# Kernel tuning notes

Hardware: AMD Instinct MI355X
Metric: run time of the kernel (lower is better)

The kernel has to match this reference:

```python
import jax, jax.numpy as jnp
import numpy as np

B, S, D_MODEL, N_HEADS, D_HEAD = 2, 2048, 512, 8, 64
AMBIENT_K = -1.0
EPS = 1e-7


def log_map_origin(x, K):
    """Lorentz log map at origin, curvature K<0. x: (..., d+1) -> (..., d)."""
    c = -K
    sc = jnp.sqrt(c)
    x_t = x[..., :1]
    x_s = x[..., 1:]
    nrm = jnp.maximum(jnp.linalg.norm(x_s, axis=-1, keepdims=True), EPS)
    theta = jnp.arccosh(jnp.maximum(sc * x_t, 1.0 + EPS)) / sc  # geodesic distance
    return theta * x_s / nrm


def exp_map_batched(u, K_vals):
    """Per-head Lorentz exp map at origin. u: (B,S,H,dh), K_vals: (H,) negative.
    Returns (B,S,H,dh+1) with time component first."""
    c = (-K_vals)[None, None, :, None]          # (1,1,H,1)
    sc = jnp.sqrt(c)
    n = jnp.maximum(jnp.linalg.norm(u, axis=-1, keepdims=True), EPS)
    t = jnp.cosh(sc * n) / sc                   # time component
    s = jnp.sinh(sc * n) / (sc * n) * u         # space components
    return jnp.concatenate([t, s], axis=-1)


def setup_inputs() -> dict:
    key = jax.random.key(0)
    k_x, k_q, k_k, k_v, k_o = jax.random.split(key, 5)
    # Lorentz points on the K=-1 manifold: x_t = sqrt(1 + |x_s|^2)
    x_s = 0.5 * jax.random.normal(k_x, (B, S, D_MODEL), dtype=jnp.float32)
    x_t = jnp.sqrt(1.0 + jnp.sum(x_s * x_s, axis=-1, keepdims=True))
    x = jnp.concatenate([x_t, x_s], axis=-1)    # (B, S, d_model+1)
    scale = 1.0 / np.sqrt(D_MODEL)
    W_q = scale * jax.random.normal(k_q, (D_MODEL, N_HEADS * D_HEAD), dtype=jnp.float32)
    W_k = scale * jax.random.normal(k_k, (D_MODEL, N_HEADS * D_HEAD), dtype=jnp.float32)
    W_v = scale * jax.random.normal(k_v, (D_MODEL, N_HEADS * D_HEAD), dtype=jnp.float32)
    W_o = scale * jax.random.normal(k_o, (N_HEADS * D_HEAD, D_MODEL), dtype=jnp.float32)
    log_abs_K = jnp.zeros((N_HEADS,), dtype=jnp.float32)  # init_K = -1 -> log(1) = 0
    return {"x": x, "W_q": W_q, "W_k": W_k, "W_v": W_v, "W_o": W_o,
            "log_abs_K": log_abs_K}


def reference(x, W_q, W_k, W_v, W_o, log_abs_K):
    b, s, _ = x.shape
    K_vals = -jnp.exp(log_abs_K)                            # (H,) negative curvatures
    x_eu = log_map_origin(x, AMBIENT_K)                     # (B,S,D)
    Q = (x_eu @ W_q).reshape(b, s, N_HEADS, D_HEAD)
    Kp = (x_eu @ W_k).reshape(b, s, N_HEADS, D_HEAD)
    V = (x_eu @ W_v).reshape(b, s, N_HEADS, D_HEAD)
    Q_hyp = exp_map_batched(Q, K_vals).transpose(0, 2, 1, 3)   # (B,H,S,dh+1)
    K_hyp = exp_map_batched(Kp, K_vals).transpose(0, 2, 1, 3)
    V = V.transpose(0, 2, 1, 3)                                # (B,H,S,dh)
    Q_t, Q_s = Q_hyp[..., 0], Q_hyp[..., 1:]
    K_t, K_s = K_hyp[..., 0], K_hyp[..., 1:]
    # Lorentzian inner product: -q_t k_t + <q_s, k_s>
    lorentz_ip = (jnp.einsum('bhqd,bhkd->bhqk', Q_s, K_s)
                  - jnp.einsum('bhq,bhk->bhqk', Q_t, K_t))
    abs_K = jnp.exp(log_abs_K)[None, :, None, None]
    scores = abs_K * (-lorentz_ip) / np.sqrt(D_HEAD)           # (B,H,S,S)
    causal = jnp.triu(jnp.ones((s, s), dtype=bool), k=1)[None, None]
    scores = jnp.where(causal, -jnp.inf, scores)
    attn = jax.nn.softmax(scores, axis=-1)
    out = jnp.einsum('bhqk,bhkd->bhqd', attn, V)               # (B,H,S,dh)
    out = out.transpose(0, 2, 1, 3).reshape(b, s, N_HEADS * D_HEAD)
    return out @ W_o                                           # (B,S,D)
```

## Files before the change

kernel.cpp:

```cpp
#include <hip/hip_runtime.h>
#include <math.h>

#define S_LEN 2048
#define B_SZ 2
#define NH 8
#define DH 64
#define DM 512
#define MROWS 4096

typedef __attribute__((ext_vector_type(8))) short s16x8;
typedef __attribute__((ext_vector_type(4))) float fx4;
typedef __attribute__((ext_vector_type(16))) float fx16;
typedef __attribute__((ext_vector_type(4))) int ix4;

__device__ inline short f2bf(float x){
  unsigned u = __float_as_uint(x);
  u = (u + 0x7FFFu + ((u >> 16) & 1u)) >> 16;
  return (short)u;
}

__device__ inline fx4 mfma16(s16x8 a, s16x8 b, fx4 c){
  return __builtin_amdgcn_mfma_f32_16x16x32_bf16(a, b, c, 0, 0, 0);
}
__device__ inline fx16 mfma32(s16x8 a, s16x8 b, fx16 c){
  return __builtin_amdgcn_mfma_f32_32x32x16_bf16(a, b, c, 0, 0, 0);
}
__device__ inline int cvtpk(float a, float b){
  int r; asm("v_cvt_pk_bf16_f32 %0, %1, %2" : "=v"(r) : "v"(a), "v"(b)); return r;
}

#define GLL16(g, l) __builtin_amdgcn_global_load_lds((const __attribute__((address_space(1))) void*)(g), (__attribute__((address_space(3))) void*)(l), 16, 0, 0)
#define GLL4(g, l)  __builtin_amdgcn_global_load_lds((const __attribute__((address_space(1))) void*)(g), (__attribute__((address_space(3))) void*)(l), 4, 0, 0)

__global__ __launch_bounds__(256) void prep_kernel(const float* __restrict__ W0,
                                                   const float* __restrict__ W1,
                                                   const float* __restrict__ W2,
                                                   const float* __restrict__ W3,
                                                   short* __restrict__ Wt,
                                                   const float* __restrict__ x,
                                                   short* __restrict__ xeu){
  __shared__ short tile[64][66];
  __shared__ float s4[4];
  int bid = blockIdx.x;
  int t = threadIdx.x;
  if (bid < 256){
    int z = bid >> 6, rem = bid & 63;
    const float* W = (z == 0) ? W0 : (z == 1) ? W1 : (z == 2) ? W2 : W3;
    short* Wtz = Wt + (size_t)z * DM * DM;
    int n0 = (rem & 7) * 64, k0 = (rem >> 3) * 64;
    int nl = t & 63;
    #pragma unroll
    for (int p = 0; p < 16; ++p){
      int kl = (t >> 6) + p * 4;
      tile[kl][nl] = f2bf(W[(size_t)(k0 + kl) * DM + n0 + nl]);
    }
    __syncthreads();
    int kl2 = t & 63;
    #pragma unroll
    for (int p = 0; p < 16; ++p){
      int nl2 = (t >> 6) + p * 4;
      Wtz[(size_t)(n0 + nl2) * DM + k0 + kl2] = tile[kl2][nl2];
    }
  } else {
    int row = 2 * (bid - 256) + (t >> 7);
    int tl = t & 127;
    const float* xr = x + (size_t)row * (DM + 1);
    float v[4]; float ss = 0.f;
    #pragma unroll
    for (int j = 0; j < 4; ++j){
      v[j] = xr[1 + tl + 128 * j];
      ss += v[j] * v[j];
    }
    #pragma unroll
    for (int off = 1; off < 64; off <<= 1) ss += __shfl_xor(ss, off);
    if ((t & 63) == 0) s4[t >> 6] = ss;
    __syncthreads();
    int g2 = t >> 7;
    float tot = s4[2 * g2] + s4[2 * g2 + 1];
    float nrm = sqrtf(tot);
    float xt = xr[0];
    float theta = acoshf(fmaxf(xt, 1.0f + 1e-7f));
    float scl = theta / fmaxf(nrm, 1e-7f);
    #pragma unroll
    for (int j = 0; j < 4; ++j)
      xeu[(size_t)row * DM + tl + 128 * j] = f2bf(scl * v[j]);
  }
}

__global__ __launch_bounds__(256, 3) void gemm_fused_kernel(const short* __restrict__ A,
                                                            const short* __restrict__ Bt,
                                                            const float* __restrict__ labsK,
                                                            float* __restrict__ Qt,
                                                            short* __restrict__ Qs,
                                                            float* __restrict__ Kt,
                                                            short* __restrict__ Ks,
                                                            short* __restrict__ Vt){
  __shared__ __attribute__((aligned(16))) short Asm[2][128 * 64];
  __shared__ __attribute__((aligned(16))) short Bsm[2][64 * 64];
  __shared__ float nrm2s[2][128];
  const int K = DM;
  int z = blockIdx.z;
  int h = blockIdx.y;
  int n0 = h * 64, m0 = blockIdx.x * 128;
  int t = threadIdx.x;
  int w = t >> 6, lane = t & 63;
  int wm = w >> 1, wn = w & 1;
  int lg = lane >> 4, lr = lane & 15;
  const short* Btz = Bt + (size_t)z * K * DM;

  int aoff[4]; const short* asrcp[4];
  int boff[2]; const short* bsrcp[2];
  #pragma unroll
  for (int j = 0; j < 4; ++j){
    int ch = t + 256 * j;
    int r = ch >> 3, c = ch & 7;
    aoff[j] = ch * 8;
    asrcp[j] = A + (size_t)(m0 + r) * K + 8 * (c ^ (r & 7));
  }
  #pragma unroll
  for (int j = 0; j < 2; ++j){
    int ch = t + 256 * j;
    int r = ch >> 3, c = ch & 7;
    boff[j] = ch * 8;
    bsrcp[j] = Btz + (size_t)(n0 + r) * K + 8 * (c ^ (r & 7));
  }

  {
    short* ab = &Asm[0][0]; short* bb = &Bsm[0][0];
    #pragma unroll
    for (int j = 0; j < 4; ++j) GLL16(asrcp[j], ab + aoff[j]);
    #pragma unroll
    for (int j = 0; j < 2; ++j) GLL16(bsrcp[j], bb + boff[j]);
  }

  fx4 acc[4][2] = {};
  for (int ks = 0; ks < 8; ++ks){
    asm volatile("s_waitcnt vmcnt(0)" ::: "memory");
    __builtin_amdgcn_s_barrier();
    if (ks < 7){
      int nb = (ks + 1) & 1;
      short* ab = &Asm[nb][0]; short* bb = &Bsm[nb][0];
      int kk = (ks + 1) * 64;
      #pragma unroll
      for (int j = 0; j < 4; ++j) GLL16(asrcp[j] + kk, ab + aoff[j]);
      #pragma unroll
      for (int j = 0; j < 2; ++j) GLL16(bsrcp[j] + kk, bb + boff[j]);
    }
    int buf = ks & 1;
    s16x8 af[4][2], bf[2][2];
    #pragma unroll
    for (int mi = 0; mi < 4; ++mi){
      int row = wm * 64 + mi * 16 + lr;
      #pragma unroll
      for (int s = 0; s < 2; ++s)
        af[mi][s] = *(const s16x8*)&Asm[buf][row * 64 + ((4 * s + lg) ^ (row & 7)) * 8];
    }
    #pragma unroll
    for (int ni = 0; ni < 2; ++ni){
      int row = wn * 32 + ni * 16 + lr;
      #pragma unroll
      for (int s = 0; s < 2; ++s)
        bf[ni][s] = *(const s16x8*)&Bsm[buf][row * 64 + ((4 * s + lg) ^ (row & 7)) * 8];
    }
    __builtin_amdgcn_s_setprio(1);
    #pragma unroll
    for (int s = 0; s < 2; ++s)
      #pragma unroll
      for (int mi = 0; mi < 4; ++mi)
        #pragma unroll
        for (int ni = 0; ni < 2; ++ni)
          acc[mi][ni] = mfma16(af[mi][s], bf[ni][s], acc[mi][ni]);
    __builtin_amdgcn_s_setprio(0);
  }

  if (z < 2){
    #pragma unroll
    for (int mi = 0; mi < 4; ++mi)
      #pragma unroll
      for (int r = 0; r < 4; ++r){
        float prt = acc[mi][0][r] * acc[mi][0][r] + acc[mi][1][r] * acc[mi][1][r];
        prt += __shfl_xor(prt, 1);
        prt += __shfl_xor(prt, 2);
        prt += __shfl_xor(prt, 4);
        prt += __shfl_xor(prt, 8);
        if (lr == 0) nrm2s[wn][wm * 64 + mi * 16 + 4 * lg + r] = prt;
      }
    __syncthreads();
    float c  = __expf(labsK[h]);
    float sc = sqrtf(c);
    float invsc = __frcp_rn(sc);
    float a  = 0.125f * c * 1.4426950408889634f;
    float tmul = (z == 0) ? a : 1.0f;
    float vmul = (z == 0) ? -a : 1.0f;
    float* Tt = (z == 0) ? Qt : Kt;
    short* Ts = (z == 0) ? Qs : Ks;
    #pragma unroll
    for (int mi = 0; mi < 4; ++mi)
      #pragma unroll
      for (int r = 0; r < 4; ++r){
        int row_local = wm * 64 + mi * 16 + 4 * lg + r;
        float full = nrm2s[0][row_local] + nrm2s[1][row_local];
        float n = fmaxf(sqrtf(full), 1e-7f);
        float arg = sc * n;
        float e = __expf(arg), ei = __frcp_rn(e);
        float tval = tmul * 0.5f * (e + ei) * invsc;
        float vscl = vmul * 0.5f * (e - ei) * __frcp_rn(arg);
        int grow = m0 + row_local;
        int b = grow >> 11, s = grow & (S_LEN - 1);
        size_t bhs = ((size_t)(b * NH + h) * S_LEN + s);
        if (lr == 0) Tt[bhs] = tval;
        #pragma unroll
        for (int ni = 0; ni < 2; ++ni)
          Ts[bhs * DH + wn * 32 + ni * 16 + lr] = f2bf(vscl * acc[mi][ni][r]);
      }
  } else {
    short* vt = (short*)&Asm[0][0];
    __syncthreads();
    #pragma unroll
    for (int mi = 0; mi < 4; ++mi)
      #pragma unroll
      for (int ni = 0; ni < 2; ++ni)
        #pragma unroll
        for (int r = 0; r < 4; ++r){
          int row_local = wm * 64 + mi * 16 + 4 * lg + r;
          int col_local = wn * 32 + ni * 16 + lr;
          vt[col_local * 136 + row_local] = f2bf(acc[mi][ni][r]);
        }
    __syncthreads();
    int d = t >> 2, sseg = (t & 3) * 32;
    int b = m0 >> 11;
    size_t vbase = ((size_t)(b * NH + h) * DH + d) * S_LEN + (m0 & (S_LEN - 1)) + sseg;
    #pragma unroll
    for (int j = 0; j < 4; ++j){
      s16x8 val = *(const s16x8*)&vt[d * 136 + sseg + 8 * j];
      *(s16x8*)(Vt + vbase + 8 * j) = val;
    }
  }
}

__global__ __launch_bounds__(256, 3) void attn_kernel(const short* __restrict__ Qs,
                                                      const float* __restrict__ Qt,
                                                      const short* __restrict__ Ks,
                                                      const float* __restrict__ Kt,
                                                      const short* __restrict__ Vt,
                                                      float* __restrict__ Mpart,
                                                      float* __restrict__ Lpart,
                                                      float* __restrict__ Opart){
  __shared__ __attribute__((aligned(16))) short Ksm[3][4096];
  __shared__ __attribute__((aligned(16))) short Vsm[3][4096];
  __shared__ __attribute__((aligned(16))) float Ktm[3][64];

  int bx = blockIdx.x;
  int bh = bx & 15;
  int id = bx >> 4;
  int g, c;
  if (id < 4)       { g = id;                 c = 0; }
  else if (id < 12) { g = 4 + ((id - 4) >> 1);  c = (id - 4) & 1; }
  else if (id < 24) { int r = id - 12; int q3 = r / 3; g = 8 + q3; c = r - 3 * q3; }
  else              { g = 12 + ((id - 24) >> 2); c = (id - 24) & 3; }
  int kbeg = 512 * c;
  int kend = 512 * c + 512; { int ge = 128 * g + 128; if (ge < kend) kend = ge; }
  int ntc = (kend - kbeg) >> 6;

  int tid = threadIdx.x;
  int w = tid >> 6, lane = tid & 63;
  int l5 = lane & 31, hi = lane >> 5;
  size_t bhS = (size_t)bh * S_LEN;

  const short* Kg  = Ks + bhS * DH;
  const short* Vg  = Vt + (size_t)bh * DH * S_LEN;
  const float* Ktg = Kt + bhS;

  int srow = lane >> 3;
  int scol = ((lane & 7) * 8) ^ (srow << 3);
  const short* kg0 = Kg + (size_t)(kbeg + 16 * w + srow) * DH + scol;
  const short* kg1 = kg0 + 8 * DH;
  const short* vg0 = Vg + (size_t)(16 * w + srow) * S_LEN + kbeg + scol;
  const short* vg1 = vg0 + 8 * S_LEN;
  const float* ktg = Ktg + kbeg + lane;

  int q0w = 128 * g + 32 * w;
  int q   = q0w + l5;
  int qmax = q0w + 31;
  s16x8 qf[4];
  #pragma unroll
  for (int dblk = 0; dblk < 4; ++dblk)
    qf[dblk] = *(const s16x8*)(Qs + (bhS + q) * DH + dblk * 16 + hi * 8);
  float aqt = Qt[bhS + q];

  fx16 acc0, acc1;
  #pragma unroll
  for (int i = 0; i < 16; ++i){ acc0[i] = 0.f; acc1[i] = 0.f; }
  float mrun = 0.f, lrun = 0.f;

  #define STAGE_T(tt, b) { int off_ = (tt) * 64; \
    GLL16(kg0 + (size_t)off_ * DH, &Ksm[b][16 * w * 64]); \
    GLL16(kg1 + (size_t)off_ * DH, &Ksm[b][16 * w * 64 + 512]); \
    GLL16(vg0 + off_, &Vsm[b][16 * w * 64]); \
    GLL16(vg1 + off_, &Vsm[b][16 * w * 64 + 512]); \
    if (w == 3) GLL4(ktg + off_, &Ktm[b][0]); }

  STAGE_T(0, 0);
  if (ntc > 1) STAGE_T(1, 1);

  int buf = 0, sbuf = 2;
  for (int t = 0; t < ntc; ++t){
    int k0 = kbeg + t * 64;
    if (t + 1 < ntc){
      if (w == 3) asm volatile("s_waitcnt vmcnt(5)" ::: "memory");
      else        asm volatile("s_waitcnt vmcnt(4)" ::: "memory");
    } else {
      asm volatile("s_waitcnt vmcnt(0)" ::: "memory");
    }
    __builtin_amdgcn_s_barrier();
    if (t + 2 < ntc) STAGE_T(t + 2, sbuf);

    if (k0 <= qmax){
      fx16 st[2];
      __builtin_amdgcn_s_setprio(1);
      #pragma unroll
      for (int s = 0; s < 2; ++s){
        const short* kb = &Ksm[buf][(32 * s + l5) * 64];
        fx16 z;
        #pragma unroll
        for (int i = 0; i < 16; ++i) z[i] = 0.f;
        #pragma unroll
        for (int dblk = 0; dblk < 4; ++dblk){
          s16x8 kf = *(const s16x8*)(kb + ((16 * dblk + 8 * hi) ^ ((l5 & 7) << 3)));
          z = mfma32(kf, qf[dblk], z);
        }
        st[s] = z;
      }
      __builtin_amdgcn_s_setprio(0);
      float p[2][16];
      #pragma unroll
      for (int s = 0; s < 2; ++s)
        #pragma unroll
        for (int m4 = 0; m4 < 4; ++m4){
          fx4 kt4 = *(const fx4*)&Ktm[buf][32 * s + 8 * m4 + 4 * hi];
          #pragma unroll
          for (int tt = 0; tt < 4; ++tt)
            p[s][4 * m4 + tt] = st[s][4 * m4 + tt] + aqt * kt4[tt];
        }
      if (k0 + 63 > q0w){
        #pragma unroll
        for (int s = 0; s < 2; ++s)
          #pragma unroll
          for (int r = 0; r < 16; ++r){
            int kg2 = k0 + 32 * s + (r & 3) + 8 * (r >> 2) + 4 * hi;
            if (kg2 > q) p[s][r] = -3e38f;
          }
      }
      float v16[16];
      #pragma unroll
      for (int i = 0; i < 16; ++i) v16[i] = fmaxf(p[0][i], p[1][i]);
      #pragma unroll
      for (int i = 0; i < 8; ++i) v16[i] = fmaxf(v16[i], v16[i + 8]);
      #pragma unroll
      for (int i = 0; i < 4; ++i) v16[i] = fmaxf(v16[i], v16[i + 4]);
      float pmax = fmaxf(fmaxf(v16[0], v16[1]), fmaxf(v16[2], v16[3]));
      pmax = fmaxf(pmax, __shfl_xor(pmax, 32));
      if (!__all(pmax <= mrun + 8.f)){
        float mnew = fmaxf(mrun, pmax);
        float scl = __builtin_amdgcn_exp2f(mrun - mnew);
        mrun = mnew;
        lrun *= scl;
        #pragma unroll
        for (int i = 0; i < 16; ++i){ acc0[i] *= scl; acc1[i] *= scl; }
      }
      float sm[16];
      #pragma unroll
      for (int i = 0; i < 16; ++i){
        p[0][i] = __builtin_amdgcn_exp2f(p[0][i] - mrun);
        p[1][i] = __builtin_amdgcn_exp2f(p[1][i] - mrun);
        sm[i] = p[0][i] + p[1][i];
      }
      #pragma unroll
      for (int i = 0; i < 8; ++i) sm[i] += sm[i + 8];
      #pragma unroll
      for (int i = 0; i < 4; ++i) sm[i] += sm[i + 4];
      float rsum = (sm[0] + sm[1]) + (sm[2] + sm[3]);
      rsum += __shfl_xor(rsum, 32);
      lrun += rsum;

      #pragma unroll
      for (int h = 0; h < 4; ++h){
        int s = h >> 1, hb = h & 1;
        int w0 = cvtpk(p[s][8 * hb + 0], p[s][8 * hb + 1]);
        int w1 = cvtpk(p[s][8 * hb + 2], p[s][8 * hb + 3]);
        int w2 = cvtpk(p[s][8 * hb + 4], p[s][8 * hb + 5]);
        int w3 = cvtpk(p[s][8 * hb + 6], p[s][8 * hb + 7]);
        int sdA = hi ? w0 : w2;
        int sdB = hi ? w1 : w3;
        int rcA = __shfl_xor(sdA, 32);
        int rcB = __shfl_xor(sdB, 32);
        ix4 fw;
        fw.x = hi ? rcA : w0; fw.y = hi ? rcB : w1;
        fw.z = hi ? w2 : rcA; fw.w = hi ? w3 : rcB;
        s16x8 pf = __builtin_bit_cast(s16x8, fw);
        const short* vb0 = &Vsm[buf][(l5) * 64 + ((16 * h + 8 * hi) ^ ((l5 & 7) << 3))];
        const short* vb1 = vb0 + 32 * 64;
        s16x8 vf0 = *(const s16x8*)vb0;
        s16x8 vf1 = *(const s16x8*)vb1;
        __builtin_amdgcn_s_setprio(1);
        acc0 = mfma32(vf0, pf, acc0);
        acc1 = mfma32(vf1, pf, acc1);
        __builtin_amdgcn_s_setprio(0);
      }
    }
    buf  = (buf == 2)  ? 0 : buf + 1;
    sbuf = (sbuf == 2) ? 0 : sbuf + 1;
  }

  int slot = ((bh << 4) + g) * 4 + c;
  int qi = 32 * w + l5;
  if (hi == 0){
    Mpart[(size_t)slot * 128 + qi] = mrun;
    Lpart[(size_t)slot * 128 + qi] = lrun;
  }
  float* Op = Opart + (size_t)slot * 8192 + (size_t)qi * 64;
  #pragma unroll
  for (int j = 0; j < 4; ++j){
    fx4 v0, v1;
    #pragma unroll
    for (int i = 0; i < 4; ++i){ v0[i] = acc0[4 * j + i]; v1[i] = acc1[4 * j + i]; }
    *(fx4*)(Op + 8 * j + 4 * hi)      = v0;
    *(fx4*)(Op + 32 + 8 * j + 4 * hi) = v1;
  }
}

__global__ __launch_bounds__(256) void combine_kernel(const float* __restrict__ Mpart,
                                                      const float* __restrict__ Lpart,
                                                      const float* __restrict__ Opart,
                                                      short* __restrict__ Obf){
  int bx = blockIdx.x;
  int bhg = bx & 255;
  int bh = bhg & 15, g = bhg >> 4;
  int qq = bx >> 8;
  int t = threadIdx.x;
  int q = qq * 32 + (t >> 3);
  int oct = t & 7;
  int nch = (g >> 2) + 1;
  int gbase = ((bh << 4) + g) * 4;

  float mc[4], lc[4];
  #pragma unroll
  for (int c = 0; c < 4; ++c){
    mc[c] = Mpart[(size_t)(gbase + c) * 128 + q];
    lc[c] = Lpart[(size_t)(gbase + c) * 128 + q];
    if (c >= nch) mc[c] = -3e38f;
  }
  float M = fmaxf(fmaxf(mc[0], mc[1]), fmaxf(mc[2], mc[3]));
  float wc[4]; float L = 0.f;
  #pragma unroll
  for (int c = 0; c < 4; ++c){
    wc[c] = __builtin_amdgcn_exp2f(mc[c] - M);
    L += wc[c] * lc[c];
  }
  float invL = 1.f / L;
  #pragma unroll
  for (int c = 0; c < 4; ++c) wc[c] *= invL;

  const float* ob = Opart + (size_t)gbase * 8192 + (size_t)q * 64 + oct * 8;
  float accf[8] = {0.f,0.f,0.f,0.f,0.f,0.f,0.f,0.f};
  #pragma unroll
  for (int c = 0; c < 4; ++c){
    fx4 a = *(const fx4*)(ob + (size_t)c * 8192);
    fx4 b = *(const fx4*)(ob + (size_t)c * 8192 + 4);
    #pragma unroll
    for (int k = 0; k < 4; ++k){ accf[k] += wc[c] * a[k]; accf[4 + k] += wc[c] * b[k]; }
  }
  s16x8 pk;
  #pragma unroll
  for (int dd = 0; dd < 8; ++dd) pk[dd] = f2bf(accf[dd]);
  int bb = bh >> 3, hh = bh & 7;
  *(s16x8*)(Obf + ((size_t)bb * S_LEN + 128 * g + q) * DM + hh * DH + oct * 8) = pk;
}

__global__ __launch_bounds__(256, 4) void gemm_o_kernel(const short* __restrict__ A,
                                                        const short* __restrict__ Bt,
                                                        float* __restrict__ C){
  __shared__ __attribute__((aligned(16))) short Asm[2][64 * 64];
  __shared__ __attribute__((aligned(16))) short Bsm[2][64 * 64];
  const int K = DM;
  int n0 = blockIdx.y * 64, m0 = blockIdx.x * 64;
  int t = threadIdx.x;
  int w = t >> 6, lane = t & 63;
  int wm = w >> 1, wn = w & 1;
  int lg = lane >> 4, lr = lane & 15;

  int aoff[2]; const short* asrcp[2];
  int boff[2]; const short* bsrcp[2];
  #pragma unroll
  for (int j = 0; j < 2; ++j){
    int ch = t + 256 * j;
    int r = ch >> 3, c = ch & 7;
    aoff[j] = ch * 8;
    asrcp[j] = A + (size_t)(m0 + r) * K + 8 * (c ^ (r & 7));
    boff[j] = ch * 8;
    bsrcp[j] = Bt + (size_t)(n0 + r) * K + 8 * (c ^ (r & 7));
  }

  {
    short* ab = &Asm[0][0]; short* bb = &Bsm[0][0];
    #pragma unroll
    for (int j = 0; j < 2; ++j){ GLL16(asrcp[j], ab + aoff[j]); GLL16(bsrcp[j], bb + boff[j]); }
  }

  fx4 acc[2][2] = {};
  for (int ks = 0; ks < 8; ++ks){
    asm volatile("s_waitcnt vmcnt(0)" ::: "memory");
    __builtin_amdgcn_s_barrier();
    if (ks < 7){
      int nb = (ks + 1) & 1;
      short* ab = &Asm[nb][0]; short* bb = &Bsm[nb][0];
      int kk = (ks + 1) * 64;
      #pragma unroll
      for (int j = 0; j < 2; ++j){ GLL16(asrcp[j] + kk, ab + aoff[j]); GLL16(bsrcp[j] + kk, bb + boff[j]); }
    }
    int buf = ks & 1;
    s16x8 af[2][2], bf[2][2];
    #pragma unroll
    for (int mi = 0; mi < 2; ++mi){
      int row = wm * 32 + mi * 16 + lr;
      #pragma unroll
      for (int s = 0; s < 2; ++s)
        af[mi][s] = *(const s16x8*)&Asm[buf][row * 64 + ((4 * s + lg) ^ (row & 7)) * 8];
    }
    #pragma unroll
    for (int ni = 0; ni < 2; ++ni){
      int row = wn * 32 + ni * 16 + lr;
      #pragma unroll
      for (int s = 0; s < 2; ++s)
        bf[ni][s] = *(const s16x8*)&Bsm[buf][row * 64 + ((4 * s + lg) ^ (row & 7)) * 8];
    }
    __builtin_amdgcn_s_setprio(1);
    #pragma unroll
    for (int s = 0; s < 2; ++s)
      #pragma unroll
      for (int mi = 0; mi < 2; ++mi)
        #pragma unroll
        for (int ni = 0; ni < 2; ++ni)
          acc[mi][ni] = mfma16(af[mi][s], bf[ni][s], acc[mi][ni]);
    __builtin_amdgcn_s_setprio(0);
  }

  #pragma unroll
  for (int mi = 0; mi < 2; ++mi)
    #pragma unroll
    for (int ni = 0; ni < 2; ++ni)
      #pragma unroll
      for (int r = 0; r < 4; ++r){
        int row = m0 + wm * 32 + mi * 16 + 4 * lg + r;
        int col = n0 + wn * 32 + ni * 16 + lr;
        C[(size_t)row * DM + col] = acc[mi][ni][r];
      }
}

extern "C" void kernel_launch(void* const* d_in, const int* in_sizes, int n_in,
                              void* d_out, int out_size, void* d_ws, size_t ws_size,
                              hipStream_t stream) {
  const float* x     = (const float*)d_in[0];
  const float* Wq    = (const float*)d_in[1];
  const float* Wk    = (const float*)d_in[2];
  const float* Wv    = (const float*)d_in[3];
  const float* Wo    = (const float*)d_in[4];
  const float* labsK = (const float*)d_in[5];

  char* w = (char*)d_ws;
  short* Wt    = (short*)(w);
  short* xeu   = (short*)(w + (2ull  << 20));
  short* Qs    = (short*)(w + (30ull << 20));
  short* Ks    = (short*)(w + (34ull << 20));
  short* Vt    = (short*)(w + (38ull << 20));
  float* Qt    = (float*)(w + (42ull << 20));
  float* Kt    = (float*)(w + (42ull << 20) + (128ull << 10));
  short* Obf   = (short*)(w + (42ull << 20) + (256ull << 10));
  float* Opart = (float*)(w + (48ull << 20));
  float* Mpart = (float*)(w + (80ull << 20));
  float* Lpart = (float*)(w + (81ull << 20));

  prep_kernel<<<dim3(2304), 256, 0, stream>>>(Wq, Wk, Wv, Wo, Wt, x, xeu);

  gemm_fused_kernel<<<dim3(32, 8, 3), 256, 0, stream>>>(
      xeu, Wt, labsK, Qt, Qs, Kt, Ks, Vt);

  attn_kernel<<<dim3(640), 256, 0, stream>>>(
      Qs, Qt, Ks, Kt, Vt, Mpart, Lpart, Opart);

  combine_kernel<<<dim3(1024), 256, 0, stream>>>(Mpart, Lpart, Opart, Obf);

  gemm_o_kernel<<<dim3(64, 8), 256, 0, stream>>>(Obf, Wt + 3 * DM * DM, (float*)d_out);
}
```

Before: 65.86 us.

## Widen QKV GEMM tiles, store normalized bf16 partials, skip combine for single-chunk groups

```diff
diff --git a/kernel.cpp b/kernel.cpp
--- a/kernel.cpp
+++ b/kernel.cpp
@@ -12,11 +12,15 @@
 typedef __attribute__((ext_vector_type(4))) float fx4;
 typedef __attribute__((ext_vector_type(16))) float fx16;
 typedef __attribute__((ext_vector_type(4))) int ix4;
+typedef __attribute__((ext_vector_type(2))) int ix2;
 
 __device__ inline short f2bf(float x){
   unsigned u = __float_as_uint(x);
   u = (u + 0x7FFFu + ((u >> 16) & 1u)) >> 16;
   return (short)u;
+}
+__device__ inline float bf2f(short s){
+  return __uint_as_float(((unsigned)(unsigned short)s) << 16);
 }
 
 __device__ inline fx4 mfma16(s16x8 a, s16x8 b, fx4 c){
@@ -40,7 +44,6 @@
                                                    const float* __restrict__ x,
                                                    short* __restrict__ xeu){
   __shared__ short tile[64][66];
-  __shared__ float s4[4];
   int bid = blockIdx.x;
   int t = threadIdx.x;
   if (bid < 256){
@@ -62,32 +65,29 @@
       Wtz[(size_t)(n0 + nl2) * DM + k0 + kl2] = tile[kl2][nl2];
     }
   } else {
-    int row = 2 * (bid - 256) + (t >> 7);
-    int tl = t & 127;
+    int row = (bid - 256) * 4 + (t >> 6);
+    int lane = t & 63;
     const float* xr = x + (size_t)row * (DM + 1);
-    float v[4]; float ss = 0.f;
-    #pragma unroll
-    for (int j = 0; j < 4; ++j){
-      v[j] = xr[1 + tl + 128 * j];
+    float v[8]; float ss = 0.f;
+    #pragma unroll
+    for (int j = 0; j < 8; ++j){
+      v[j] = xr[1 + lane * 8 + j];
       ss += v[j] * v[j];
     }
     #pragma unroll
     for (int off = 1; off < 64; off <<= 1) ss += __shfl_xor(ss, off);
-    if ((t & 63) == 0) s4[t >> 6] = ss;
-    __syncthreads();
-    int g2 = t >> 7;
-    float tot = s4[2 * g2] + s4[2 * g2 + 1];
-    float nrm = sqrtf(tot);
+    float nrm = sqrtf(ss);
     float xt = xr[0];
     float theta = acoshf(fmaxf(xt, 1.0f + 1e-7f));
     float scl = theta / fmaxf(nrm, 1e-7f);
-    #pragma unroll
-    for (int j = 0; j < 4; ++j)
-      xeu[(size_t)row * DM + tl + 128 * j] = f2bf(scl * v[j]);
-  }
-}
-
-__global__ __launch_bounds__(256, 3) void gemm_fused_kernel(const short* __restrict__ A,
+    s16x8 pk;
+    #pragma unroll
+    for (int j = 0; j < 8; ++j) pk[j] = f2bf(scl * v[j]);
+    *(s16x8*)(xeu + (size_t)row * DM + lane * 8) = pk;
+  }
+}
+
+__global__ __launch_bounds__(256, 2) void gemm_fused_kernel(const short* __restrict__ A,
                                                             const short* __restrict__ Bt,
                                                             const float* __restrict__ labsK,
                                                             float* __restrict__ Qt,
@@ -95,72 +95,65 @@
                                                             float* __restrict__ Kt,
                                                             short* __restrict__ Ks,
                                                             short* __restrict__ Vt){
-  __shared__ __attribute__((aligned(16))) short Asm[2][128 * 64];
-  __shared__ __attribute__((aligned(16))) short Bsm[2][64 * 64];
-  __shared__ float nrm2s[2][128];
+  __shared__ __attribute__((aligned(16))) short Stage[4][8192];
   const int K = DM;
   int z = blockIdx.z;
-  int h = blockIdx.y;
-  int n0 = h * 64, m0 = blockIdx.x * 128;
+  int hp = blockIdx.y;
+  int n0 = hp * 128, m0 = blockIdx.x * 128;
   int t = threadIdx.x;
   int w = t >> 6, lane = t & 63;
   int wm = w >> 1, wn = w & 1;
   int lg = lane >> 4, lr = lane & 15;
   const short* Btz = Bt + (size_t)z * K * DM;
 
-  int aoff[4]; const short* asrcp[4];
-  int boff[2]; const short* bsrcp[2];
+  int coff[4]; const short* asrcp[4]; const short* bsrcp[4];
   #pragma unroll
   for (int j = 0; j < 4; ++j){
     int ch = t + 256 * j;
     int r = ch >> 3, c = ch & 7;
-    aoff[j] = ch * 8;
-    asrcp[j] = A + (size_t)(m0 + r) * K + 8 * (c ^ (r & 7));
-  }
-  #pragma unroll
-  for (int j = 0; j < 2; ++j){
-    int ch = t + 256 * j;
-    int r = ch >> 3, c = ch & 7;
-    boff[j] = ch * 8;
+    coff[j] = ch * 8;
+    asrcp[j] = A   + (size_t)(m0 + r) * K + 8 * (c ^ (r & 7));
     bsrcp[j] = Btz + (size_t)(n0 + r) * K + 8 * (c ^ (r & 7));
   }
 
-  {
-    short* ab = &Asm[0][0]; short* bb = &Bsm[0][0];
-    #pragma unroll
-    for (int j = 0; j < 4; ++j) GLL16(asrcp[j], ab + aoff[j]);
-    #pragma unroll
-    for (int j = 0; j < 2; ++j) GLL16(bsrcp[j], bb + boff[j]);
-  }
-
-  fx4 acc[4][2] = {};
+  #pragma unroll
+  for (int j = 0; j < 4; ++j){
+    GLL16(asrcp[j], &Stage[0][coff[j]]);
+    GLL16(bsrcp[j], &Stage[2][coff[j]]);
+  }
+
+  fx4 acc[4][4] = {};
+  for (int ks = 0; ks < 4; ++ks){
+    ;
+    break;
+  }
   for (int ks = 0; ks < 8; ++ks){
     asm volatile("s_waitcnt vmcnt(0)" ::: "memory");
     __builtin_amdgcn_s_barrier();
     if (ks < 7){
       int nb = (ks + 1) & 1;
-      short* ab = &Asm[nb][0]; short* bb = &Bsm[nb][0];
       int kk = (ks + 1) * 64;
       #pragma unroll
-      for (int j = 0; j < 4; ++j) GLL16(asrcp[j] + kk, ab + aoff[j]);
-      #pragma unroll
-      for (int j = 0; j < 2; ++j) GLL16(bsrcp[j] + kk, bb + boff[j]);
+      for (int j = 0; j < 4; ++j){
+        GLL16(asrcp[j] + kk, &Stage[nb][coff[j]]);
+        GLL16(bsrcp[j] + kk, &Stage[2 + nb][coff[j]]);
+      }
     }
     int buf = ks & 1;
-    s16x8 af[4][2], bf[2][2];
+    s16x8 af[4][2], bf[4][2];
     #pragma unroll
     for (int mi = 0; mi < 4; ++mi){
       int row = wm * 64 + mi * 16 + lr;
       #pragma unroll
       for (int s = 0; s < 2; ++s)
-        af[mi][s] = *(const s16x8*)&Asm[buf][row * 64 + ((4 * s + lg) ^ (row & 7)) * 8];
-    }
-    #pragma unroll
-    for (int ni = 0; ni < 2; ++ni){
-      int row = wn * 32 + ni * 16 + lr;
+        af[mi][s] = *(const s16x8*)&Stage[buf][row * 64 + ((4 * s + lg) ^ (row & 7)) * 8];
+    }
+    #pragma unroll
+    for (int ni = 0; ni < 4; ++ni){
+      int row = wn * 64 + ni * 16 + lr;
       #pragma unroll
       for (int s = 0; s < 2; ++s)
-        bf[ni][s] = *(const s16x8*)&Bsm[buf][row * 64 + ((4 * s + lg) ^ (row & 7)) * 8];
+        bf[ni][s] = *(const s16x8*)&Stage[2 + buf][row * 64 + ((4 * s + lg) ^ (row & 7)) * 8];
     }
     __builtin_amdgcn_s_setprio(1);
     #pragma unroll
@@ -168,24 +161,13 @@
       #pragma unroll
       for (int mi = 0; mi < 4; ++mi)
         #pragma unroll
-        for (int ni = 0; ni < 2; ++ni)
+        for (int ni = 0; ni < 4; ++ni)
           acc[mi][ni] = mfma16(af[mi][s], bf[ni][s], acc[mi][ni]);
     __builtin_amdgcn_s_setprio(0);
   }
 
+  int h = hp * 2 + wn;
   if (z < 2){
-    #pragma unroll
-    for (int mi = 0; mi < 4; ++mi)
-      #pragma unroll
-      for (int r = 0; r < 4; ++r){
-        float prt = acc[mi][0][r] * acc[mi][0][r] + acc[mi][1][r] * acc[mi][1][r];
-        prt += __shfl_xor(prt, 1);
-        prt += __shfl_xor(prt, 2);
-        prt += __shfl_xor(prt, 4);
-        prt += __shfl_xor(prt, 8);
-        if (lr == 0) nrm2s[wn][wm * 64 + mi * 16 + 4 * lg + r] = prt;
-      }
-    __syncthreads();
     float c  = __expf(labsK[h]);
     float sc = sqrtf(c);
     float invsc = __frcp_rn(sc);
@@ -198,42 +180,43 @@
     for (int mi = 0; mi < 4; ++mi)
       #pragma unroll
       for (int r = 0; r < 4; ++r){
-        int row_local = wm * 64 + mi * 16 + 4 * lg + r;
-        float full = nrm2s[0][row_local] + nrm2s[1][row_local];
-        float n = fmaxf(sqrtf(full), 1e-7f);
+        float prt = 0.f;
+        #pragma unroll
+        for (int ni = 0; ni < 4; ++ni) prt += acc[mi][ni][r] * acc[mi][ni][r];
+        prt += __shfl_xor(prt, 1);
+        prt += __shfl_xor(prt, 2);
+        prt += __shfl_xor(prt, 4);
+        prt += __shfl_xor(prt, 8);
+        float n = fmaxf(sqrtf(prt), 1e-7f);
         float arg = sc * n;
         float e = __expf(arg), ei = __frcp_rn(e);
         float tval = tmul * 0.5f * (e + ei) * invsc;
         float vscl = vmul * 0.5f * (e - ei) * __frcp_rn(arg);
-        int grow = m0 + row_local;
+        int grow = m0 + wm * 64 + mi * 16 + 4 * lg + r;
         int b = grow >> 11, s = grow & (S_LEN - 1);
         size_t bhs = ((size_t)(b * NH + h) * S_LEN + s);
         if (lr == 0) Tt[bhs] = tval;
         #pragma unroll
-        for (int ni = 0; ni < 2; ++ni)
-          Ts[bhs * DH + wn * 32 + ni * 16 + lr] = f2bf(vscl * acc[mi][ni][r]);
+        for (int ni = 0; ni < 4; ++ni)
+          Ts[bhs * DH + ni * 16 + lr] = f2bf(vscl * acc[mi][ni][r]);
       }
   } else {
-    short* vt = (short*)&Asm[0][0];
     __syncthreads();
+    short* vt = &Stage[0][0] + w * 4352;
     #pragma unroll
     for (int mi = 0; mi < 4; ++mi)
       #pragma unroll
-      for (int ni = 0; ni < 2; ++ni)
-        #pragma unroll
-        for (int r = 0; r < 4; ++r){
-          int row_local = wm * 64 + mi * 16 + 4 * lg + r;
-          int col_local = wn * 32 + ni * 16 + lr;
-          vt[col_local * 136 + row_local] = f2bf(acc[mi][ni][r]);
-        }
-    __syncthreads();
-    int d = t >> 2, sseg = (t & 3) * 32;
+      for (int ni = 0; ni < 4; ++ni)
+        #pragma unroll
+        for (int r = 0; r < 4; ++r)
+          vt[(ni * 16 + lr) * 68 + mi * 16 + 4 * lg + r] = f2bf(acc[mi][ni][r]);
     int b = m0 >> 11;
-    size_t vbase = ((size_t)(b * NH + h) * DH + d) * S_LEN + (m0 & (S_LEN - 1)) + sseg;
-    #pragma unroll
-    for (int j = 0; j < 4; ++j){
-      s16x8 val = *(const s16x8*)&vt[d * 136 + sseg + 8 * j];
-      *(s16x8*)(Vt + vbase + 8 * j) = val;
+    int sglob = (m0 & (S_LEN - 1)) + wm * 64;
+    size_t vbase = ((size_t)(b * NH + h) * DH + lane) * S_LEN + sglob;
+    #pragma unroll
+    for (int j = 0; j < 8; ++j){
+      s16x8 val = *(const s16x8*)&vt[lane * 68 + j * 8];
+      *(s16x8*)(Vt + vbase + j * 8) = val;
     }
   }
 }
@@ -245,7 +228,8 @@
                                                       const short* __restrict__ Vt,
                                                       float* __restrict__ Mpart,
                                                       float* __restrict__ Lpart,
-                                                      float* __restrict__ Opart){
+                                                      short* __restrict__ Obn,
+                                                      short* __restrict__ Obf){
   __shared__ __attribute__((aligned(16))) short Ksm[3][4096];
   __shared__ __attribute__((aligned(16))) short Vsm[3][4096];
   __shared__ __attribute__((aligned(16))) float Ktm[3][64];
@@ -258,6 +242,7 @@
   else if (id < 12) { g = 4 + ((id - 4) >> 1);  c = (id - 4) & 1; }
   else if (id < 24) { int r = id - 12; int q3 = r / 3; g = 8 + q3; c = r - 3 * q3; }
   else              { g = 12 + ((id - 24) >> 2); c = (id - 24) & 3; }
+  int nch = (g >> 2) + 1;
   int kbeg = 512 * c;
   int kend = 512 * c + 512; { int ge = 128 * g + 128; if (ge < kend) kend = ge; }
   int ntc = (kend - kbeg) >> 6;
@@ -412,31 +397,50 @@
     sbuf = (sbuf == 2) ? 0 : sbuf + 1;
   }
 
-  int slot = ((bh << 4) + g) * 4 + c;
+  float invl = 1.0f / lrun;
   int qi = 32 * w + l5;
-  if (hi == 0){
-    Mpart[(size_t)slot * 128 + qi] = mrun;
-    Lpart[(size_t)slot * 128 + qi] = lrun;
-  }
-  float* Op = Opart + (size_t)slot * 8192 + (size_t)qi * 64;
-  #pragma unroll
-  for (int j = 0; j < 4; ++j){
-    fx4 v0, v1;
-    #pragma unroll
-    for (int i = 0; i < 4; ++i){ v0[i] = acc0[4 * j + i]; v1[i] = acc1[4 * j + i]; }
-    *(fx4*)(Op + 8 * j + 4 * hi)      = v0;
-    *(fx4*)(Op + 32 + 8 * j + 4 * hi) = v1;
+  if (nch == 1){
+    int bb = bh >> 3, hh = bh & 7;
+    short* orow = Obf + ((size_t)bb * S_LEN + 128 * g + qi) * DM + hh * DH;
+    #pragma unroll
+    for (int j = 0; j < 4; ++j){
+      ix2 v0, v1;
+      v0.x = cvtpk(acc0[4 * j + 0] * invl, acc0[4 * j + 1] * invl);
+      v0.y = cvtpk(acc0[4 * j + 2] * invl, acc0[4 * j + 3] * invl);
+      v1.x = cvtpk(acc1[4 * j + 0] * invl, acc1[4 * j + 1] * invl);
+      v1.y = cvtpk(acc1[4 * j + 2] * invl, acc1[4 * j + 3] * invl);
+      *(ix2*)(orow + 8 * j + 4 * hi)      = v0;
+      *(ix2*)(orow + 32 + 8 * j + 4 * hi) = v1;
+    }
+  } else {
+    int slot = ((bh << 4) + g) * 4 + c;
+    if (hi == 0){
+      Mpart[(size_t)slot * 128 + qi] = mrun;
+      Lpart[(size_t)slot * 128 + qi] = lrun;
+    }
+    short* Op = Obn + (size_t)slot * 8192 + (size_t)qi * 64;
+    #pragma unroll
+    for (int j = 0; j < 4; ++j){
+      ix2 v0, v1;
+      v0.x = cvtpk(acc0[4 * j + 0] * invl, acc0[4 * j + 1] * invl);
+      v0.y = cvtpk(acc0[4 * j + 2] * invl, acc0[4 * j + 3] * invl);
+      v1.x = cvtpk(acc1[4 * j + 0] * invl, acc1[4 * j + 1] * invl);
+      v1.y = cvtpk(acc1[4 * j + 2] * invl, acc1[4 * j + 3] * invl);
+      *(ix2*)(Op + 8 * j + 4 * hi)      = v0;
+      *(ix2*)(Op + 32 + 8 * j + 4 * hi) = v1;
+    }
   }
 }
 
 __global__ __launch_bounds__(256) void combine_kernel(const float* __restrict__ Mpart,
                                                       const float* __restrict__ Lpart,
-                                                      const float* __restrict__ Opart,
+                                                      const short* __restrict__ Obn,
                                                       short* __restrict__ Obf){
   int bx = blockIdx.x;
-  int bhg = bx & 255;
-  int bh = bhg & 15, g = bhg >> 4;
-  int qq = bx >> 8;
+  int bhg = bx % 192;
+  int qq = bx / 192;
+  int bh = bhg & 15;
+  int g = 4 + (bhg >> 4);
   int t = threadIdx.x;
   int q = qq * 32 + (t >> 3);
   int oct = t & 7;
@@ -451,24 +455,24 @@
     if (c >= nch) mc[c] = -3e38f;
   }
   float M = fmaxf(fmaxf(mc[0], mc[1]), fmaxf(mc[2], mc[3]));
-  float wc[4]; float L = 0.f;
+  float ww[4]; float D = 0.f;
   #pragma unroll
   for (int c = 0; c < 4; ++c){
-    wc[c] = __builtin_amdgcn_exp2f(mc[c] - M);
-    L += wc[c] * lc[c];
-  }
-  float invL = 1.f / L;
-  #pragma unroll
-  for (int c = 0; c < 4; ++c) wc[c] *= invL;
-
-  const float* ob = Opart + (size_t)gbase * 8192 + (size_t)q * 64 + oct * 8;
+    ww[c] = __builtin_amdgcn_exp2f(mc[c] - M) * lc[c];
+    if (c >= nch) ww[c] = 0.f;
+    D += ww[c];
+  }
+  float invD = 1.f / D;
+  #pragma unroll
+  for (int c = 0; c < 4; ++c) ww[c] *= invD;
+
+  const short* ob = Obn + (size_t)gbase * 8192 + (size_t)q * 64 + oct * 8;
   float accf[8] = {0.f,0.f,0.f,0.f,0.f,0.f,0.f,0.f};
   #pragma unroll
   for (int c = 0; c < 4; ++c){
-    fx4 a = *(const fx4*)(ob + (size_t)c * 8192);
-    fx4 b = *(const fx4*)(ob + (size_t)c * 8192 + 4);
-    #pragma unroll
-    for (int k = 0; k < 4; ++k){ accf[k] += wc[c] * a[k]; accf[4 + k] += wc[c] * b[k]; }
+    s16x8 v = *(const s16x8*)(ob + (size_t)c * 8192);
+    #pragma unroll
+    for (int i = 0; i < 8; ++i) accf[i] += ww[c] * bf2f(v[i]);
   }
   s16x8 pk;
   #pragma unroll
@@ -576,19 +580,19 @@
   float* Qt    = (float*)(w + (42ull << 20));
   float* Kt    = (float*)(w + (42ull << 20) + (128ull << 10));
   short* Obf   = (short*)(w + (42ull << 20) + (256ull << 10));
-  float* Opart = (float*)(w + (48ull << 20));
+  short* Obn   = (short*)(w + (48ull << 20));
   float* Mpart = (float*)(w + (80ull << 20));
   float* Lpart = (float*)(w + (81ull << 20));
 
-  prep_kernel<<<dim3(2304), 256, 0, stream>>>(Wq, Wk, Wv, Wo, Wt, x, xeu);
-
-  gemm_fused_kernel<<<dim3(32, 8, 3), 256, 0, stream>>>(
+  prep_kernel<<<dim3(1280), 256, 0, stream>>>(Wq, Wk, Wv, Wo, Wt, x, xeu);
+
+  gemm_fused_kernel<<<dim3(32, 4, 3), 256, 0, stream>>>(
       xeu, Wt, labsK, Qt, Qs, Kt, Ks, Vt);
 
   attn_kernel<<<dim3(640), 256, 0, stream>>>(
-      Qs, Qt, Ks, Kt, Vt, Mpart, Lpart, Opart);
-
-  combine_kernel<<<dim3(1024), 256, 0, stream>>>(Mpart, Lpart, Opart, Obf);
+      Qs, Qt, Ks, Kt, Vt, Mpart, Lpart, Obn, Obf);
+
+  combine_kernel<<<dim3(768), 256, 0, stream>>>(Mpart, Lpart, Obn, Obf);
 
   gemm_o_kernel<<<dim3(64, 8), 256, 0, stream>>>(Obf, Wt + 3 * DM * DM, (float*)d_out);
 }
```

New measurement: 59.86 us. -9.1%, faster.
